# Performance work log

Hardware: AMD Instinct MI355X
Metric: run time of the kernel (lower is better)

The kernel has to match this reference:

```python
import jax, jax.numpy as jnp
import numpy as np

DEPTH = 5
HID = 128
NODE_F = 16
OUT_F = 1
N_NODES = 25000
N_EDGES = 200000
N_GRAPHS = 64


def _lin(key, fan_in, fan_out):
    k1, k2 = jax.random.split(key)
    lim = 1.0 / np.sqrt(fan_in)
    W = jax.random.uniform(k1, (fan_in, fan_out), minval=-lim, maxval=lim, dtype=jnp.float32)
    b = jax.random.uniform(k2, (fan_out,), minval=-lim, maxval=lim, dtype=jnp.float32)
    return W, b


def _stack_lin(key, fan_in, fan_out):
    Ws, bs = zip(*[_lin(k, fan_in, fan_out) for k in jax.random.split(key, DEPTH)])
    return jnp.stack(Ws), jnp.stack(bs)


def setup_inputs() -> dict:
    key = jax.random.key(0)
    ks = jax.random.split(key, 12)
    inp = {}
    inp["x"] = jax.random.normal(ks[0], (N_NODES, NODE_F), dtype=jnp.float32)
    inp["pos"] = jax.random.normal(ks[1], (N_NODES, 3), dtype=jnp.float32)
    inp["edge_index"] = jax.random.randint(ks[2], (2, N_EDGES), 0, N_NODES)
    inp["batch"] = jnp.sort(jax.random.randint(ks[3], (N_NODES,), 0, N_GRAPHS))
    inp["emb_W"], inp["emb_b"] = _lin(ks[4], NODE_F, HID)
    inp["msg_W1"], inp["msg_b1"] = _stack_lin(ks[5], 2 * HID + 1, HID)
    inp["msg_W2"], inp["msg_b2"] = _stack_lin(ks[6], HID, HID)
    inp["upd_W1"], inp["upd_b1"] = _stack_lin(ks[7], 2 * HID, HID)
    inp["upd_W2"], inp["upd_b2"] = _stack_lin(ks[8], HID, HID)
    ones = jnp.ones((DEPTH, HID), jnp.float32)
    zeros = jnp.zeros((DEPTH, HID), jnp.float32)
    inp["msg_g1"], inp["msg_be1"] = ones, zeros
    inp["msg_g2"], inp["msg_be2"] = ones, zeros
    inp["upd_g1"], inp["upd_be1"] = ones, zeros
    inp["upd_g2"], inp["upd_be2"] = ones, zeros
    inp["pred_W1"], inp["pred_b1"] = _lin(ks[9], HID, HID)
    inp["pred_W2"], inp["pred_b2"] = _lin(ks[10], HID, OUT_F)
    return inp


def _ln(v, g, b, eps=1e-5):
    m = jnp.mean(v, axis=-1, keepdims=True)
    var = jnp.mean((v - m) ** 2, axis=-1, keepdims=True)
    return (v - m) * jax.lax.rsqrt(var + eps) * g + b


def reference(x, pos, edge_index, batch,
              emb_W, emb_b,
              msg_W1, msg_b1, msg_g1, msg_be1, msg_W2, msg_b2, msg_g2, msg_be2,
              upd_W1, upd_b1, upd_g1, upd_be1, upd_W2, upd_b2, upd_g2, upd_be2,
              pred_W1, pred_b1, pred_W2, pred_b2):
    src, dst = edge_index[0], edge_index[1]
    # pos is never updated in EGNN_Full.forward, so distances are constant
    dists = jnp.linalg.norm(pos[dst] - pos[src], axis=-1, keepdims=True)  # [E,1]
    h = x @ emb_W + emb_b  # [N,HID]
    for l in range(DEPTH):
        m = jnp.concatenate([h[dst], h[src], dists], axis=-1)  # [E, 2*HID+1]
        m = jax.nn.relu(_ln(m @ msg_W1[l] + msg_b1[l], msg_g1[l], msg_be1[l]))
        m = jax.nn.relu(_ln(m @ msg_W2[l] + msg_b2[l], msg_g2[l], msg_be2[l]))
        agg = jax.ops.segment_sum(m, dst, num_segments=N_NODES)  # [N,HID]
        u = jnp.concatenate([h, agg], axis=-1)  # [N, 2*HID]
        u = jax.nn.relu(_ln(u @ upd_W1[l] + upd_b1[l], upd_g1[l], upd_be1[l]))
        u = jax.nn.relu(_ln(u @ upd_W2[l] + upd_b2[l], upd_g2[l], upd_be2[l]))
        h = h + u  # residual
    g = jax.ops.segment_sum(h, batch, num_segments=N_GRAPHS)  # global_add_pool
    return jax.nn.relu(g @ pred_W1 + pred_b1) @ pred_W2 + pred_b2  # [G, OUT_F]
```

## Files before the change

kernel.cpp:

```cpp
#include <hip/hip_runtime.h>
#include <hip/hip_bf16.h>

#define N_NODES 25000
#define N_EDGES 200000
#define N_GRAPHS 64
#define HID 128
#define DEPTH 5

typedef _Float16 half8 __attribute__((ext_vector_type(8)));
typedef _Float16 half2v __attribute__((ext_vector_type(2)));
typedef float f32x4 __attribute__((ext_vector_type(4)));

__device__ inline half8 pack8(float4 a, float4 b) {
    half8 r;
    r[0] = (_Float16)a.x; r[1] = (_Float16)a.y; r[2] = (_Float16)a.z; r[3] = (_Float16)a.w;
    r[4] = (_Float16)b.x; r[5] = (_Float16)b.y; r[6] = (_Float16)b.z; r[7] = (_Float16)b.w;
    return r;
}

__global__ void embed_kernel(const float* __restrict__ x, const float* __restrict__ W,
                             const float* __restrict__ b, float* __restrict__ h) {
    for (int i = blockIdx.x * blockDim.x + threadIdx.x; i < N_NODES * HID;
         i += gridDim.x * blockDim.x) {
        int n = i >> 7, j = i & 127;
        float acc = b[j];
        #pragma unroll
        for (int k = 0; k < 16; k++) acc += x[n * 16 + k] * W[k * 128 + j];
        h[i] = acc;
    }
}

__global__ void prep_kernel(const float* __restrict__ msg_W1, const float* __restrict__ msg_W2,
                            const float* __restrict__ upd_W1, const float* __restrict__ upd_W2,
                            _Float16* __restrict__ usW, _Float16* __restrict__ eW2,
                            _Float16* __restrict__ uW1, _Float16* __restrict__ uW2) {
    int i = blockIdx.x * blockDim.x + threadIdx.x;
    const int N_US = DEPTH * 32768, N_E2 = DEPTH * 16384, N_U1 = DEPTH * 32768, N_U2 = DEPTH * 16384;
    if (i < N_US) {
        int l = i >> 15, r = i & 32767;
        int j = r & 7, low6 = (r >> 3) & 63, kq = (low6 >> 4) & 3, s_ = low6 & 15;
        int rest = r >> 9, tt = rest & 15, kb = rest >> 4;
        int kk = (kb << 5) | (kq << 3) | j;
        int uh = tt >> 3, t = tt & 7, cc = s_ * 8 + t;
        const float* W1 = msg_W1 + (size_t)l * 257 * 128;
        usW[i] = (_Float16)(uh ? W1[(128 + kk) * 128 + cc] : W1[kk * 128 + cc]);
        return;
    }
    i -= N_US;
    if (i < N_E2) {
        int l = i >> 14, r = i & 16383;
        int j = r & 7, low6 = (r >> 3) & 63, kq = (low6 >> 4) & 3, s_ = low6 & 15;
        int rest = r >> 9, t = rest & 7, kb = rest >> 3;
        int k = (kb << 5) | (kq << 3) | j, c = s_ * 8 + t;
        eW2[i] = (_Float16)msg_W2[(size_t)l * 16384 + k * 128 + c];
        return;
    }
    i -= N_E2;
    if (i < N_U1) {
        int l = i >> 15, r = i & 32767;
        int j = r & 7, low6 = (r >> 3) & 63, kq = (low6 >> 4) & 3, s_ = low6 & 15;
        int rest = r >> 9, t = rest & 7, kb = rest >> 3;
        int k = (kb << 5) | (kq << 3) | j, c = s_ * 8 + t;
        uW1[i] = (_Float16)upd_W1[(size_t)l * 32768 + k * 128 + c];
        return;
    }
    i -= N_U1;
    if (i < N_U2) {
        int l = i >> 14, r = i & 16383;
        int j = r & 7, low6 = (r >> 3) & 63, kq = (low6 >> 4) & 3, s_ = low6 & 15;
        int rest = r >> 9, t = rest & 7, kb = rest >> 3;
        int k = (kb << 5) | (kq << 3) | j, c = s_ * 8 + t;
        uW2[i] = (_Float16)upd_W2[(size_t)l * 16384 + k * 128 + c];
    }
}

__global__ void hist_kernel(const int* __restrict__ ei, int* __restrict__ cnt) {
    int e = blockIdx.x * blockDim.x + threadIdx.x;
    if (e < N_EDGES) atomicAdd(&cnt[ei[N_EDGES + e]], 1);
}

__global__ __launch_bounds__(1024)
void scan_kernel(const int* cnt, int* rowptr, int* cursor) {
    __shared__ int swsum[16];
    __shared__ int stot;
    const int tid = threadIdx.x, wave = tid >> 6, lane = tid & 63;
    int carry = 0;
    for (int base = 0; base < N_NODES; base += 1024) {
        int i = base + tid;
        int v0 = (i < N_NODES) ? cnt[i] : 0;
        int v = v0;
        #pragma unroll
        for (int d = 1; d < 64; d <<= 1) {
            int t = __shfl_up(v, d, 64);
            if (lane >= d) v += t;
        }
        if (lane == 63) swsum[wave] = v;
        __syncthreads();
        if (wave == 0) {
            int sv = (lane < 16) ? swsum[lane] : 0;
            int si = sv;
            #pragma unroll
            for (int d = 1; d < 16; d <<= 1) {
                int t = __shfl_up(si, d, 64);
                if (lane >= d) si += t;
            }
            if (lane < 16) swsum[lane] = si - sv;
            if (lane == 15) stot = si;
        }
        __syncthreads();
        int excl = v - v0 + swsum[wave] + carry;
        if (i < N_NODES) { rowptr[i] = excl; cursor[i] = excl; }
        carry += stot;
        __syncthreads();
    }
    if (tid == 0) rowptr[N_NODES] = carry;
}

__global__ void scatter_kernel(const int* __restrict__ ei, const float* __restrict__ pos,
                               int* __restrict__ cursor, int* __restrict__ src_s,
                               int* __restrict__ dst_s, float* __restrict__ dist_s) {
    int e = blockIdx.x * blockDim.x + threadIdx.x;
    if (e < N_EDGES) {
        int s = ei[e], d = ei[N_EDGES + e];
        int p = atomicAdd(&cursor[d], 1);
        src_s[p] = s; dst_s[p] = d;
        float dx = pos[d * 3 + 0] - pos[s * 3 + 0];
        float dy = pos[d * 3 + 1] - pos[s * 3 + 1];
        float dz = pos[d * 3 + 2] - pos[s * 3 + 2];
        dist_s[p] = sqrtf(dx * dx + dy * dy + dz * dz);
    }
}

__global__ __launch_bounds__(512, 2)
void us_kernel(const float* __restrict__ h, const _Float16* __restrict__ Wf,
               const float* __restrict__ bias1,
               _Float16* __restrict__ U, _Float16* __restrict__ S,
               float* __restrict__ agg) {
    __shared__ __attribute__((aligned(16))) _Float16 sW[32768];
    __shared__ float sB1[128];
    const int tid = threadIdx.x;
    {
        const half8* wsrc = (const half8*)Wf;
        half8* wdst = (half8*)sW;
        #pragma unroll
        for (int idx = tid; idx < 4096; idx += 512) wdst[idx] = wsrc[idx];
    }
    if (tid < 128) sB1[tid] = bias1[tid];
    __syncthreads();

    const int w = tid >> 6, lane = tid & 63, quad = lane >> 4, s = lane & 15;
    float b1c[8];
    #pragma unroll
    for (int t = 0; t < 8; t++) b1c[t] = sB1[s * 8 + t];

    const int gw = blockIdx.x * 8 + w, nwaves = gridDim.x * 8;
    const int nwt = (N_NODES + 15) >> 4;
    for (int wt = gw; wt < nwt; wt += nwaves) {
        const int nbase = wt << 4;
        int n = nbase + s; if (n >= N_NODES) n = N_NODES - 1;

        half8 af[4];
        #pragma unroll
        for (int kb = 0; kb < 4; kb++) {
            const float* rp = h + (size_t)n * 128 + kb * 32 + quad * 8;
            af[kb] = pack8(*(const float4*)rp, *(const float4*)(rp + 4));
        }

        #pragma unroll
        for (int uhalf = 0; uhalf < 2; uhalf++) {
            f32x4 acc[8];
            #pragma unroll
            for (int t = 0; t < 8; t++) { f32x4 z = {0.f, 0.f, 0.f, 0.f}; acc[t] = z; }
            #pragma unroll
            for (int kb = 0; kb < 4; kb++) {
                #pragma unroll
                for (int t = 0; t < 8; t++) {
                    half8 bf = *(const half8*)(&sW[((((kb << 4) + (uhalf * 8 + t)) << 6) + lane) * 8]);
                    acc[t] = __builtin_amdgcn_mfma_f32_16x16x32_f16(af[kb], bf, acc[t], 0, 0, 0);
                }
            }
            _Float16* dstbuf = uhalf ? S : U;
            #pragma unroll
            for (int r = 0; r < 4; r++) {
                int nn = nbase + quad * 4 + r;
                if (nn < N_NODES) {
                    half8 ov;
                    #pragma unroll
                    for (int t = 0; t < 8; t++)
                        ov[t] = (_Float16)(acc[t][r] + (uhalf ? 0.f : b1c[t]));
                    *(half8*)(&dstbuf[(size_t)nn * 128 + s * 8]) = ov;
                    if (uhalf == 0) {
                        float4 z4 = {0.f, 0.f, 0.f, 0.f};
                        float* ap = agg + (size_t)nn * 128 + s * 8;
                        *(float4*)ap = z4;
                        *(float4*)(ap + 4) = z4;
                    }
                }
            }
        }
    }
}

__global__ __launch_bounds__(256, 2)
void edge_kernel(const _Float16* __restrict__ U, const _Float16* __restrict__ S,
                 const float* __restrict__ dist_s, const int* __restrict__ src_s,
                 const int* __restrict__ dst_s,
                 const float* __restrict__ w256, const float* __restrict__ gam1,
                 const float* __restrict__ bet1,
                 const _Float16* __restrict__ W2f, const float* __restrict__ bias2,
                 const float* __restrict__ gam2, const float* __restrict__ bet2,
                 float* __restrict__ agg) {
    __shared__ __attribute__((aligned(16))) _Float16 sW2[16384];
    __shared__ _Float16 sM1[17408];
    __shared__ int   sDstA[4][34];
    __shared__ int   sSrcA[4][32];
    __shared__ float sDistA[4][32];
    __shared__ float sB[768];

    const int tid = threadIdx.x;
    {
        const half8* wsrc = (const half8*)W2f;
        half8* wdst = (half8*)sW2;
        #pragma unroll
        for (int idx = tid; idx < 2048; idx += 256) wdst[idx] = wsrc[idx];
    }
    if (tid < 128) {
        sB[tid] = w256[tid];
        sB[128 + tid] = gam1[tid]; sB[256 + tid] = bet1[tid];
        sB[384 + tid] = bias2[tid]; sB[512 + tid] = gam2[tid]; sB[640 + tid] = bet2[tid];
    }
    __syncthreads();

    const int w = tid >> 6, lane = tid & 63, quad = lane >> 4, s = lane & 15;
    _Float16* myM1 = &sM1[w * (32 * 136)];
    int*   sDst  = sDstA[w];
    int*   sSrc  = sSrcA[w];
    float* sDist = sDistA[w];

    float w256c[8], g1c[8], be1c[8], b2c[8], g2c[8], be2c[8];
    #pragma unroll
    for (int t = 0; t < 8; t++) {
        int c = s * 8 + t;
        w256c[t] = sB[c]; g1c[t] = sB[128 + c]; be1c[t] = sB[256 + c];
        b2c[t] = sB[384 + c]; g2c[t] = sB[512 + c]; be2c[t] = sB[640 + c];
    }

    const int gw = blockIdx.x * 4 + w, nwaves = gridDim.x * 4;
    const int ewt = N_EDGES >> 5;
    for (int wt = gw; wt < ewt; wt += nwaves) {
        const int ebase = wt << 5;

        if (lane <= 32) {
            int e = ebase + lane;
            sDst[lane] = (e < N_EDGES) ? dst_s[e] : -1;
        } else {
            sSrc[lane - 33] = src_s[ebase + lane - 33];
        }
        if (lane < 32) sDist[lane] = dist_s[ebase + lane];
        else if (lane == 32) sSrc[31] = src_s[ebase + 31];
        bool bnd = (lane < 32) && (sDst[lane] != sDst[lane + 1]);
        unsigned mask = (unsigned)(__ballot(bnd) & 0xffffffffull);
        mask |= 0x80000000u;

        float distA[8];
        half8 u8A[8], s8A[8];
        #pragma unroll
        for (int i = 0; i < 8; i++) {
            int row = (i >> 2) * 16 + quad * 4 + (i & 3);
            int d = sDst[row], si = sSrc[row];
            distA[i] = sDist[row];
            u8A[i] = *(const half8*)(&U[(size_t)d * 128 + s * 8]);
            s8A[i] = *(const half8*)(&S[(size_t)si * 128 + s * 8]);
        }

        #pragma unroll
        for (int i = 0; i < 8; i++) {
            float v[8], sum = 0.f, sq = 0.f;
            #pragma unroll
            for (int t = 0; t < 8; t++) {
                v[t] = (float)u8A[i][t] + (float)s8A[i][t] + distA[i] * w256c[t];
                sum += v[t]; sq += v[t] * v[t];
            }
            #pragma unroll
            for (int m = 1; m < 16; m <<= 1) {
                sum += __shfl_xor(sum, m, 64);
                sq  += __shfl_xor(sq, m, 64);
            }
            float mean = sum * (1.f / 128.f);
            float var = sq * (1.f / 128.f) - mean * mean;
            float rstd = rsqrtf(var + 1e-5f);
            half8 hv;
            #pragma unroll
            for (int t = 0; t < 8; t++) {
                float y = (v[t] - mean) * rstd * g1c[t] + be1c[t];
                hv[t] = (_Float16)fmaxf(y, 0.f);
            }
            *(half8*)(&myM1[((i >> 2) * 16 + quad * 4 + (i & 3)) * 136 + s * 8]) = hv;
        }

        f32x4 acc2[2][8];
        #pragma unroll
        for (int mt = 0; mt < 2; mt++)
            #pragma unroll
            for (int t = 0; t < 8; t++) { f32x4 z = {0.f, 0.f, 0.f, 0.f}; acc2[mt][t] = z; }
        #pragma unroll
        for (int kb = 0; kb < 4; kb++) {
            half8 af[2];
            #pragma unroll
            for (int mt = 0; mt < 2; mt++)
                af[mt] = *(const half8*)(&myM1[(mt * 16 + s) * 136 + kb * 32 + quad * 8]);
            #pragma unroll
            for (int t = 0; t < 8; t++) {
                half8 bf = *(const half8*)(&sW2[(((kb << 3) + t) * 64 + lane) * 8]);
                acc2[0][t] = __builtin_amdgcn_mfma_f32_16x16x32_f16(af[0], bf, acc2[0][t], 0, 0, 0);
                acc2[1][t] = __builtin_amdgcn_mfma_f32_16x16x32_f16(af[1], bf, acc2[1][t], 0, 0, 0);
            }
        }

        #pragma unroll
        for (int mt = 0; mt < 2; mt++) {
            #pragma unroll
            for (int r = 0; r < 4; r++) {
                float v[8], sum = 0.f, sq = 0.f;
                #pragma unroll
                for (int t = 0; t < 8; t++) {
                    v[t] = acc2[mt][t][r] + b2c[t];
                    sum += v[t]; sq += v[t] * v[t];
                }
                #pragma unroll
                for (int m = 1; m < 16; m <<= 1) {
                    sum += __shfl_xor(sum, m, 64);
                    sq  += __shfl_xor(sq, m, 64);
                }
                float mean = sum * (1.f / 128.f);
                float var = sq * (1.f / 128.f) - mean * mean;
                float rstd = rsqrtf(var + 1e-5f);
                half8 hv;
                #pragma unroll
                for (int t = 0; t < 8; t++) {
                    float y = (v[t] - mean) * rstd * g2c[t] + be2c[t];
                    hv[t] = (_Float16)fmaxf(y, 0.f);
                }
                *(half8*)(&myM1[(mt * 16 + quad * 4 + r) * 136 + s * 8]) = hv;
            }
        }

        {
            const int col2 = lane * 2;
            half2v acc; acc[0] = (_Float16)0.f; acc[1] = (_Float16)0.f;
            for (int row = 0; row < 32; row++) {
                half2v v = *(const half2v*)(&myM1[row * 136 + col2]);
                acc += v;
                if ((mask >> row) & 1u) {
                    int d = sDst[row];
                    float a0 = (float)acc[0], a1 = (float)acc[1];
                    if (a0 != 0.f) atomicAdd(&agg[(size_t)d * 128 + col2], a0);
                    if (a1 != 0.f) atomicAdd(&agg[(size_t)d * 128 + col2 + 1], a1);
                    acc[0] = (_Float16)0.f; acc[1] = (_Float16)0.f;
                }
            }
        }
    }
}

__global__ __launch_bounds__(512, 1)
void upd_kernel(float* __restrict__ h, float* __restrict__ agg,
                const _Float16* __restrict__ W1f, const float* __restrict__ bias1,
                const float* __restrict__ gam1, const float* __restrict__ bet1,
                const _Float16* __restrict__ W2f, const float* __restrict__ bias2,
                const float* __restrict__ gam2, const float* __restrict__ bet2,
                const _Float16* __restrict__ usWf, const float* __restrict__ nb1,
                _Float16* __restrict__ U, _Float16* __restrict__ S, int do_us) {
    __shared__ __attribute__((aligned(16))) _Float16 sW1[32768];
    __shared__ __attribute__((aligned(16))) _Float16 sW2[16384];
    __shared__ _Float16 sM1[17408];
    __shared__ float sB[768];

    const int tid = threadIdx.x;
    {
        const half8* w1src = (const half8*)W1f;
        half8* w1dst = (half8*)sW1;
        #pragma unroll
        for (int idx = tid; idx < 4096; idx += 512) w1dst[idx] = w1src[idx];
        const half8* w2src = (const half8*)W2f;
        half8* w2dst = (half8*)sW2;
        #pragma unroll
        for (int idx = tid; idx < 2048; idx += 512) w2dst[idx] = w2src[idx];
    }
    if (tid < 128) {
        sB[tid] = bias1[tid]; sB[128 + tid] = gam1[tid]; sB[256 + tid] = bet1[tid];
        sB[384 + tid] = bias2[tid]; sB[512 + tid] = gam2[tid]; sB[640 + tid] = bet2[tid];
    }
    __syncthreads();

    const int w = tid >> 6, lane = tid & 63, quad = lane >> 4, s = lane & 15;
    _Float16* myM1 = &sM1[w * (16 * 136)];

    const int wt = blockIdx.x * 8 + w;
    const int nwt = (N_NODES + 15) >> 4;
    const bool active = (wt < nwt);
    const int nbase = wt << 4;

    if (active) {
        float b1c[8], g1c[8], be1c[8], b2c[8], g2c[8], be2c[8];
        #pragma unroll
        for (int t = 0; t < 8; t++) {
            int c = s * 8 + t;
            b1c[t] = sB[c]; g1c[t] = sB[128 + c]; be1c[t] = sB[256 + c];
            b2c[t] = sB[384 + c]; g2c[t] = sB[512 + c]; be2c[t] = sB[640 + c];
        }
        int n = nbase + s; if (n >= N_NODES) n = N_NODES - 1;

        f32x4 acc[8];
        #pragma unroll
        for (int t = 0; t < 8; t++) { f32x4 z = {0.f, 0.f, 0.f, 0.f}; acc[t] = z; }
        #pragma unroll
        for (int kb = 0; kb < 8; kb++) {
            const float* rp = (kb < 4) ? (h + (size_t)n * 128 + kb * 32 + quad * 8)
                                       : (agg + (size_t)n * 128 + (kb - 4) * 32 + quad * 8);
            half8 af = pack8(*(const float4*)rp, *(const float4*)(rp + 4));
            #pragma unroll
            for (int t = 0; t < 8; t++) {
                half8 bf = *(const half8*)(&sW1[(((kb << 3) + t) * 64 + lane) * 8]);
                acc[t] = __builtin_amdgcn_mfma_f32_16x16x32_f16(af, bf, acc[t], 0, 0, 0);
            }
        }

        #pragma unroll
        for (int r = 0; r < 4; r++) {
            float v[8], sum = 0.f, sq = 0.f;
            #pragma unroll
            for (int t = 0; t < 8; t++) {
                v[t] = acc[t][r] + b1c[t];
                sum += v[t]; sq += v[t] * v[t];
            }
            #pragma unroll
            for (int m = 1; m < 16; m <<= 1) {
                sum += __shfl_xor(sum, m, 64);
                sq  += __shfl_xor(sq, m, 64);
            }
            float mean = sum * (1.f / 128.f);
            float var = sq * (1.f / 128.f) - mean * mean;
            float rstd = rsqrtf(var + 1e-5f);
            half8 hv;
            #pragma unroll
            for (int t = 0; t < 8; t++) {
                float y = (v[t] - mean) * rstd * g1c[t] + be1c[t];
                hv[t] = (_Float16)fmaxf(y, 0.f);
            }
            *(half8*)(&myM1[(quad * 4 + r) * 136 + s * 8]) = hv;
        }

        f32x4 acc2[8];
        #pragma unroll
        for (int t = 0; t < 8; t++) { f32x4 z = {0.f, 0.f, 0.f, 0.f}; acc2[t] = z; }
        #pragma unroll
        for (int kb = 0; kb < 4; kb++) {
            half8 af = *(const half8*)(&myM1[s * 136 + kb * 32 + quad * 8]);
            #pragma unroll
            for (int t = 0; t < 8; t++) {
                half8 bf = *(const half8*)(&sW2[(((kb << 3) + t) * 64 + lane) * 8]);
                acc2[t] = __builtin_amdgcn_mfma_f32_16x16x32_f16(af, bf, acc2[t], 0, 0, 0);
            }
        }

        #pragma unroll
        for (int r = 0; r < 4; r++) {
            int nn = nbase + quad * 4 + r;
            float v[8], sum = 0.f, sq = 0.f;
            #pragma unroll
            for (int t = 0; t < 8; t++) {
                v[t] = acc2[t][r] + b2c[t];
                sum += v[t]; sq += v[t] * v[t];
            }
            #pragma unroll
            for (int m = 1; m < 16; m <<= 1) {
                sum += __shfl_xor(sum, m, 64);
                sq  += __shfl_xor(sq, m, 64);
            }
            float mean = sum * (1.f / 128.f);
            float var = sq * (1.f / 128.f) - mean * mean;
            float rstd = rsqrtf(var + 1e-5f);
            if (nn < N_NODES) {
                float* hp = h + (size_t)nn * 128 + s * 8;
                float4 h0 = *(float4*)hp;
                float4 h1 = *(float4*)(hp + 4);
                float hn[8];
                #pragma unroll
                for (int t = 0; t < 8; t++) {
                    float u = (v[t] - mean) * rstd * g2c[t] + be2c[t];
                    hn[t] = fmaxf(u, 0.f);
                }
                h0.x += hn[0]; h0.y += hn[1]; h0.z += hn[2]; h0.w += hn[3];
                h1.x += hn[4]; h1.y += hn[5]; h1.z += hn[6]; h1.w += hn[7];
                *(float4*)hp = h0;
                *(float4*)(hp + 4) = h1;
                half8 hv = pack8(h0, h1);
                *(half8*)(&myM1[(quad * 4 + r) * 136 + s * 8]) = hv;
            }
        }
    }

    if (do_us) {
        __syncthreads();
        {
            const half8* wsrc = (const half8*)usWf;
            half8* wdst = (half8*)sW1;
            #pragma unroll
            for (int idx = tid; idx < 4096; idx += 512) wdst[idx] = wsrc[idx];
        }
        __syncthreads();
        if (active) {
            float nb1c[8];
            #pragma unroll
            for (int t = 0; t < 8; t++) nb1c[t] = nb1[s * 8 + t];
            half8 af[4];
            #pragma unroll
            for (int kb = 0; kb < 4; kb++)
                af[kb] = *(const half8*)(&myM1[s * 136 + kb * 32 + quad * 8]);
            #pragma unroll
            for (int uhalf = 0; uhalf < 2; uhalf++) {
                f32x4 acc[8];
                #pragma unroll
                for (int t = 0; t < 8; t++) { f32x4 z = {0.f, 0.f, 0.f, 0.f}; acc[t] = z; }
                #pragma unroll
                for (int kb = 0; kb < 4; kb++) {
                    #pragma unroll
                    for (int t = 0; t < 8; t++) {
                        half8 bf = *(const half8*)(&sW1[((((kb << 4) + (uhalf * 8 + t)) << 6) + lane) * 8]);
                        acc[t] = __builtin_amdgcn_mfma_f32_16x16x32_f16(af[kb], bf, acc[t], 0, 0, 0);
                    }
                }
                _Float16* dstbuf = uhalf ? S : U;
                #pragma unroll
                for (int r = 0; r < 4; r++) {
                    int nn = nbase + quad * 4 + r;
                    if (nn < N_NODES) {
                        half8 ov;
                        #pragma unroll
                        for (int t = 0; t < 8; t++)
                            ov[t] = (_Float16)(acc[t][r] + (uhalf ? 0.f : nb1c[t]));
                        *(half8*)(&dstbuf[(size_t)nn * 128 + s * 8]) = ov;
                        if (uhalf == 0) {
                            float4 z4 = {0.f, 0.f, 0.f, 0.f};
                            float* ap = agg + (size_t)nn * 128 + s * 8;
                            *(float4*)ap = z4;
                            *(float4*)(ap + 4) = z4;
                        }
                    }
                }
            }
        }
    }
}

__global__ void pool_kernel(const float* __restrict__ h, const int* __restrict__ batch,
                            float* __restrict__ g) {
    const int CHUNK = 125;
    int blo = blockIdx.x * CHUNK;
    int bhi = blo + CHUNK; if (bhi > N_NODES) bhi = N_NODES;
    int j = threadIdx.x & 127;
    int half = threadIdx.x >> 7;
    float acc = 0.f; int cur = -1;
    for (int n = blo + half; n < bhi; n += 2) {
        int b = batch[n];
        if (b != cur) {
            if (cur >= 0) atomicAdd(&g[cur * 128 + j], acc);
            cur = b; acc = 0.f;
        }
        acc += h[(size_t)n * 128 + j];
    }
    if (cur >= 0) atomicAdd(&g[cur * 128 + j], acc);
}

__global__ void pred_kernel(const float* __restrict__ g, const float* __restrict__ W1,
                            const float* __restrict__ b1, const float* __restrict__ W2,
                            const float* __restrict__ b2, float* __restrict__ out) {
    int b = blockIdx.x, j = threadIdx.x;
    float t = b1[j];
    for (int k = 0; k < 128; k++) t += g[b * 128 + k] * W1[k * 128 + j];
    t = fmaxf(t, 0.f);
    __shared__ float red[128];
    red[j] = t * W2[j];
    __syncthreads();
    for (int off = 64; off > 0; off >>= 1) {
        if (j < off) red[j] += red[j + off];
        __syncthreads();
    }
    if (j == 0) out[b] = red[0] + b2[0];
}

extern "C" void kernel_launch(void* const* d_in, const int* in_sizes, int n_in,
                              void* d_out, int out_size, void* d_ws, size_t ws_size,
                              hipStream_t stream) {
    const float* x      = (const float*)d_in[0];
    const float* pos    = (const float*)d_in[1];
    const int*   ei     = (const int*)d_in[2];
    const int*   batch  = (const int*)d_in[3];
    const float* emb_W  = (const float*)d_in[4];
    const float* emb_b  = (const float*)d_in[5];
    const float* msg_W1 = (const float*)d_in[6];
    const float* msg_b1 = (const float*)d_in[7];
    const float* msg_W2 = (const float*)d_in[8];
    const float* msg_b2 = (const float*)d_in[9];
    const float* upd_W1 = (const float*)d_in[10];
    const float* upd_b1 = (const float*)d_in[11];
    const float* upd_W2 = (const float*)d_in[12];
    const float* upd_b2 = (const float*)d_in[13];
    const float* msg_g1 = (const float*)d_in[14];
    const float* msg_be1= (const float*)d_in[15];
    const float* msg_g2 = (const float*)d_in[16];
    const float* msg_be2= (const float*)d_in[17];
    const float* upd_g1 = (const float*)d_in[18];
    const float* upd_be1= (const float*)d_in[19];
    const float* upd_g2 = (const float*)d_in[20];
    const float* upd_be2= (const float*)d_in[21];
    const float* pred_W1= (const float*)d_in[22];
    const float* pred_b1= (const float*)d_in[23];
    const float* pred_W2= (const float*)d_in[24];
    const float* pred_b2= (const float*)d_in[25];
    float* out = (float*)d_out;

    float* ws = (float*)d_ws;
    float*     h      = ws;
    _Float16*  U      = (_Float16*)(ws + 3200000);
    _Float16*  S      = (_Float16*)(ws + 4800000);
    float*     agg    = ws + 6400000;
    _Float16*  usW    = (_Float16*)(ws + 9600000);
    _Float16*  eW2    = usW + DEPTH * 32768;
    _Float16*  uW1    = eW2 + DEPTH * 16384;
    _Float16*  uW2    = uW1 + DEPTH * 32768;
    int*       rowptr = (int*)(ws + 19200000);
    int*       cursor = rowptr + 25008;
    int*       src_s  = cursor + 25008;
    int*       dst_s  = src_s + 200000;
    float*     dist_s = (float*)(dst_s + 200000);
    float*     g      = dist_s + 200000;

    hipMemsetAsync(cursor, 0, 25001 * sizeof(int), stream);
    hist_kernel<<<(N_EDGES + 255) / 256, 256, 0, stream>>>(ei, cursor);
    scan_kernel<<<1, 1024, 0, stream>>>(cursor, rowptr, cursor);
    scatter_kernel<<<(N_EDGES + 255) / 256, 256, 0, stream>>>(ei, pos, cursor, src_s, dst_s, dist_s);
    prep_kernel<<<1920, 256, 0, stream>>>(msg_W1, msg_W2, upd_W1, upd_W2, usW, eW2, uW1, uW2);

    embed_kernel<<<4096, 256, 0, stream>>>(x, emb_W, emb_b, h);

    us_kernel<<<256, 512, 0, stream>>>(h, usW, msg_b1, U, S, agg);

    for (int l = 0; l < DEPTH; l++) {
        const float* W1l = msg_W1 + (size_t)l * 257 * 128;
        edge_kernel<<<512, 256, 0, stream>>>(
            U, S, dist_s, src_s, dst_s,
            W1l + 256 * 128, msg_g1 + l * 128, msg_be1 + l * 128,
            eW2 + (size_t)l * 16384, msg_b2 + l * 128, msg_g2 + l * 128, msg_be2 + l * 128,
            agg);
        int do_us = (l + 1 < DEPTH) ? 1 : 0;
        int ln = (l + 1 < DEPTH) ? (l + 1) : 0;
        upd_kernel<<<256, 512, 0, stream>>>(
            h, agg,
            uW1 + (size_t)l * 32768, upd_b1 + l * 128, upd_g1 + l * 128, upd_be1 + l * 128,
            uW2 + (size_t)l * 16384, upd_b2 + l * 128, upd_g2 + l * 128, upd_be2 + l * 128,
            usW + (size_t)ln * 32768, msg_b1 + ln * 128, U, S, do_us);
    }

    hipMemsetAsync(g, 0, N_GRAPHS * 128 * sizeof(float), stream);
    pool_kernel<<<200, 256, 0, stream>>>(h, batch, g);
    pred_kernel<<<64, 128, 0, stream>>>(g, pred_W1, pred_b1, pred_W2, pred_b2, out);
}
```

Before: 582.9 us.

## Software-pipeline edge tile gathers in edge kernel with double-buffered indices

The edge kernel now prefetches the next tile's dst/src/dist indices into a second shared buffer, then issues the gathers of U/S rows for that tile before the MFMA stage of the current tile. The aim is to hide global gather latency behind the matmul and LayerNorm work. It holds an extra 8 half8 pairs plus distances in registers, which raises register pressure under launch_bounds(256,2) and may cause spills or lower occupancy.

```diff
diff --git a/kernel.cpp b/kernel.cpp
--- a/kernel.cpp
+++ b/kernel.cpp
@@ -212,9 +212,9 @@
                  float* __restrict__ agg) {
     __shared__ __attribute__((aligned(16))) _Float16 sW2[16384];
     __shared__ _Float16 sM1[17408];
-    __shared__ int   sDstA[4][34];
-    __shared__ int   sSrcA[4][32];
-    __shared__ float sDistA[4][32];
+    __shared__ int   sDstA[4][2][34];
+    __shared__ int   sSrcA[4][2][32];
+    __shared__ float sDistA[4][2][32];
     __shared__ float sB[768];
 
     const int tid = threadIdx.x;
@@ -233,9 +233,6 @@
 
     const int w = tid >> 6, lane = tid & 63, quad = lane >> 4, s = lane & 15;
     _Float16* myM1 = &sM1[w * (32 * 136)];
-    int*   sDst  = sDstA[w];
-    int*   sSrc  = sSrcA[w];
-    float* sDist = sDistA[w];
 
     float w256c[8], g1c[8], be1c[8], b2c[8], g2c[8], be2c[8];
     #pragma unroll
@@ -247,30 +244,50 @@
 
     const int gw = blockIdx.x * 4 + w, nwaves = gridDim.x * 4;
     const int ewt = N_EDGES >> 5;
-    for (int wt = gw; wt < ewt; wt += nwaves) {
-        const int ebase = wt << 5;
-
+
+    int wt = gw;
+    int buf = 0;
+    unsigned mask_cur = 0;
+    float distA[8];
+    half8 u8A[8], s8A[8];
+
+    if (wt < ewt) {
+        const int eb = wt << 5;
         if (lane <= 32) {
-            int e = ebase + lane;
-            sDst[lane] = (e < N_EDGES) ? dst_s[e] : -1;
+            int e = eb + lane;
+            sDstA[w][0][lane] = (e < N_EDGES) ? dst_s[e] : -1;
         } else {
-            sSrc[lane - 33] = src_s[ebase + lane - 33];
-        }
-        if (lane < 32) sDist[lane] = dist_s[ebase + lane];
-        else if (lane == 32) sSrc[31] = src_s[ebase + 31];
-        bool bnd = (lane < 32) && (sDst[lane] != sDst[lane + 1]);
-        unsigned mask = (unsigned)(__ballot(bnd) & 0xffffffffull);
-        mask |= 0x80000000u;
-
-        float distA[8];
-        half8 u8A[8], s8A[8];
+            sSrcA[w][0][lane - 33] = src_s[eb + lane - 33];
+        }
+        if (lane < 32) sDistA[w][0][lane] = dist_s[eb + lane];
+        else if (lane == 32) sSrcA[w][0][31] = src_s[eb + 31];
+        bool bnd = (lane < 32) && (sDstA[w][0][lane] != sDstA[w][0][lane + 1]);
+        mask_cur = (unsigned)(__ballot(bnd) & 0xffffffffull) | 0x80000000u;
         #pragma unroll
         for (int i = 0; i < 8; i++) {
             int row = (i >> 2) * 16 + quad * 4 + (i & 3);
-            int d = sDst[row], si = sSrc[row];
-            distA[i] = sDist[row];
+            int d = sDstA[w][0][row], si = sSrcA[w][0][row];
+            distA[i] = sDistA[w][0][row];
             u8A[i] = *(const half8*)(&U[(size_t)d * 128 + s * 8]);
             s8A[i] = *(const half8*)(&S[(size_t)si * 128 + s * 8]);
+        }
+    }
+
+    while (wt < ewt) {
+        const int wt_next = wt + nwaves;
+        const bool hasnext = (wt_next < ewt);
+        const int nb = buf ^ 1;
+
+        if (hasnext) {
+            const int eb = wt_next << 5;
+            if (lane <= 32) {
+                int e = eb + lane;
+                sDstA[w][nb][lane] = (e < N_EDGES) ? dst_s[e] : -1;
+            } else {
+                sSrcA[w][nb][lane - 33] = src_s[eb + lane - 33];
+            }
+            if (lane < 32) sDistA[w][nb][lane] = dist_s[eb + lane];
+            else if (lane == 32) sSrcA[w][nb][31] = src_s[eb + 31];
         }
 
         #pragma unroll
@@ -296,6 +313,22 @@
                 hv[t] = (_Float16)fmaxf(y, 0.f);
             }
             *(half8*)(&myM1[((i >> 2) * 16 + quad * 4 + (i & 3)) * 136 + s * 8]) = hv;
+        }
+
+        unsigned mask_next = 0;
+        half8 u8B[8], s8B[8];
+        float distB[8];
+        if (hasnext) {
+            bool bnd = (lane < 32) && (sDstA[w][nb][lane] != sDstA[w][nb][lane + 1]);
+            mask_next = (unsigned)(__ballot(bnd) & 0xffffffffull) | 0x80000000u;
+            #pragma unroll
+            for (int i = 0; i < 8; i++) {
+                int row = (i >> 2) * 16 + quad * 4 + (i & 3);
+                int d = sDstA[w][nb][row], si = sSrcA[w][nb][row];
+                distB[i] = sDistA[w][nb][row];
+                u8B[i] = *(const half8*)(&U[(size_t)d * 128 + s * 8]);
+                s8B[i] = *(const half8*)(&S[(size_t)si * 128 + s * 8]);
+            }
         }
 
         f32x4 acc2[2][8];
@@ -351,8 +384,8 @@
             for (int row = 0; row < 32; row++) {
                 half2v v = *(const half2v*)(&myM1[row * 136 + col2]);
                 acc += v;
-                if ((mask >> row) & 1u) {
-                    int d = sDst[row];
+                if ((mask_cur >> row) & 1u) {
+                    int d = sDstA[w][buf][row];
                     float a0 = (float)acc[0], a1 = (float)acc[1];
                     if (a0 != 0.f) atomicAdd(&agg[(size_t)d * 128 + col2], a0);
                     if (a1 != 0.f) atomicAdd(&agg[(size_t)d * 128 + col2 + 1], a1);
@@ -360,6 +393,14 @@
                 }
             }
         }
+
+        if (hasnext) {
+            #pragma unroll
+            for (int i = 0; i < 8; i++) { u8A[i] = u8B[i]; s8A[i] = s8B[i]; distA[i] = distB[i]; }
+            mask_cur = mask_next;
+        }
+        buf = nb;
+        wt = wt_next;
     }
 }
 
```

Measured after the change: 587.0 us. Within noise of the previous version (+0.7%).
